# Performance work log

Hardware: AMD Instinct MI355X
Metric: run time of the kernel (lower is better)

The kernel has to match this reference:

```python
import jax, jax.numpy as jnp
import numpy as np

ANCHORS_ALL = jnp.array([[10.,13.],[16.,30.],[33.,23.],[30.,61.],[62.,45.],
                         [59.,119.],[116.,90.],[156.,198.],[373.,326.]], dtype=jnp.float32)
INDICES = jnp.array([0, 1, 2], dtype=jnp.int32)   # anchor indices of level 0
ANCH_LVL = ANCHORS_ALL[0:3]                        # [nA, 2] anchors for this level
STRIDE = 8.0
N_CLS = 80
NA = 3


def _bce_logits(x, t):
    # elementwise binary_cross_entropy_with_logits (same formula as torch)
    return jnp.maximum(x, 0.0) - x * t + jnp.log1p(jnp.exp(-jnp.abs(x)))


def _iou_cxcywh(a, b):
    # a: [..., 4], b: [..., 4] (broadcastable), boxes as (cx, cy, w, h)
    ax1, ax2 = a[..., 0] - a[..., 2] * 0.5, a[..., 0] + a[..., 2] * 0.5
    ay1, ay2 = a[..., 1] - a[..., 3] * 0.5, a[..., 1] + a[..., 3] * 0.5
    bx1, bx2 = b[..., 0] - b[..., 2] * 0.5, b[..., 0] + b[..., 2] * 0.5
    by1, by2 = b[..., 1] - b[..., 3] * 0.5, b[..., 1] + b[..., 3] * 0.5
    iw = jnp.clip(jnp.minimum(ax2, bx2) - jnp.maximum(ax1, bx1), 0.0)
    ih = jnp.clip(jnp.minimum(ay2, by2) - jnp.maximum(ay1, by1), 0.0)
    inter = iw * ih
    union = (ax2 - ax1) * (ay2 - ay1) + (bx2 - bx1) * (by2 - by1) - inter
    return inter / (union + 1e-16)


def setup_inputs() -> dict:
    key = jax.random.key(0)
    ks = jax.random.split(key, 7)
    nB, nA, nH, nW, G = 8, 3, 160, 160, 32
    t_bbox = jax.random.normal(ks[0], (nB, nA, nH, nW, 4), jnp.float32)
    conf_logits = jax.random.normal(ks[1], (nB, nA, nH, nW, 1), jnp.float32)
    cls_logits = jax.random.normal(ks[2], (nB, nA, nH, nW, N_CLS), jnp.float32)
    cxy = jax.random.uniform(ks[3], (nB, G, 2), jnp.float32, 20.0, 1260.0)
    wh = jax.random.uniform(ks[4], (nB, G, 2), jnp.float32, 5.0, 60.0)
    gt_bboxes = jnp.concatenate([cxy, wh], axis=-1)           # cxcywh
    gt_cls = jax.random.randint(ks[5], (nB, G), 0, N_CLS, jnp.int32)
    gt_mask = jax.random.uniform(ks[6], (nB, G)) < 0.8        # padded-GT validity
    return dict(t_bbox=t_bbox, conf_logits=conf_logits, cls_logits=cls_logits,
                gt_bboxes=gt_bboxes, gt_cls=gt_cls, gt_mask=gt_mask)


def reference(t_bbox, conf_logits, cls_logits, gt_bboxes, gt_cls, gt_mask):
    nB, nA, nH, nW, _ = t_bbox.shape
    N = nA * nH * nW
    # ---- bbox decode (torch does this on a detached copy) ----
    sig = jax.nn.sigmoid(jax.lax.stop_gradient(t_bbox))
    yv, xv = jnp.meshgrid(jnp.arange(nH), jnp.arange(nW), indexing='ij')
    grid = jnp.stack([xv, yv], axis=-1).astype(jnp.float32).reshape(1, 1, nH, nW, 2)
    p_xy = (sig[..., 0:2] * 2.0 - 0.5 + grid) * STRIDE
    p_wh = (sig[..., 2:4] * 2.0) ** 2 * ANCH_LVL.reshape(1, nA, 1, 1, 2)
    p_bbox = jnp.concatenate([p_xy, p_wh], axis=-1).reshape(nB, N, 4)
    p_conf = jax.nn.sigmoid(jax.lax.stop_gradient(conf_logits))       # [nB,nA,nH,nW,1]
    p_cls = jax.nn.sigmoid(jax.lax.stop_gradient(cls_logits))
    cls_score = jnp.max(p_cls, axis=-1, keepdims=True)
    cls_idx = jnp.argmax(p_cls, axis=-1).reshape(nB, N)
    score = (p_conf * cls_score).reshape(nB, N)
    # ---- per-GT best-anchor matching (vectorized over [nB, G]) ----
    gw, gh = gt_bboxes[..., 2], gt_bboxes[..., 3]
    aw, ah = ANCHORS_ALL[:, 0], ANCHORS_ALL[:, 1]
    inter = jnp.minimum(gw[..., None], aw) * jnp.minimum(gh[..., None], ah)
    union = (gw * gh)[..., None] + aw * ah - inter
    anch_idx = jnp.argmax(inter / (union + 1e-16), axis=-1)           # [nB,G]
    matched = jnp.any(anch_idx[..., None] == INDICES, axis=-1)
    valid = gt_mask & matched
    ta = (anch_idx % NA).astype(jnp.int32)
    ti = jnp.clip((gt_bboxes[..., 0] / STRIDE).astype(jnp.int32), 0, nW - 1)
    tj = jnp.clip((gt_bboxes[..., 1] / STRIDE).astype(jnp.int32), 0, nH - 1)
    b_idx = jnp.arange(nB)[:, None]
    t_bb = t_bbox[b_idx, ta, tj, ti]       # [nB,G,4]
    t_cl = cls_logits[b_idx, ta, tj, ti]   # [nB,G,C]
    tgt_xy = ((gt_bboxes[..., 0:2] / STRIDE) % 1.0 + 0.5) / 2.0
    tgt_wh = jnp.sqrt(gt_bboxes[..., 2:4] / ANCH_LVL[ta]) / 2.0
    vm = valid.astype(t_bbox.dtype)
    loss_xy = jnp.sum(vm * jnp.sum(_bce_logits(t_bb[..., 0:2], tgt_xy), axis=-1))
    loss_wh = jnp.sum(vm * jnp.sum(_bce_logits(t_bb[..., 2:4], tgt_wh), axis=-1))
    onehot = jax.nn.one_hot(gt_cls, N_CLS, dtype=t_bbox.dtype)
    loss_cls = jnp.sum(vm * jnp.mean(_bce_logits(t_cl, onehot), axis=-1))
    # ---- objectness target: max IoU of every decoded box with the GTs ----
    ious = _iou_cxcywh(p_bbox[:, :, None, :], gt_bboxes[:, None, :, :])  # [nB,N,G]
    ious = jnp.where(gt_mask[:, None, :], ious, -1.0)
    has_gt = jnp.any(gt_mask, axis=-1)
    tconf = jnp.where(has_gt[:, None], jnp.max(ious, axis=-1), 0.0)
    tconf = tconf.reshape(nB, nA, nH, nW, 1)
    loss_conf = jnp.sum(_bce_logits(conf_logits, tconf))
    loss = (loss_xy + loss_wh + loss_conf + loss_cls) / nB
    return p_bbox, cls_idx, score, loss
```

## Files before the change

kernel.cpp:

```cpp
#include <hip/hip_runtime.h>

#define NB 8
#define NA 3
#define NH 160
#define NW 160
#define NCLS 80
#define NGT 32
#define NPB (NA * NH * NW)
#define TOTAL (NB * NPB)
#define OFF_CLSIDX (TOTAL * 4)
#define OFF_SCORE  (TOTAL * 5)
#define OFF_LOSS   (TOTAL * 6)

__device__ float g_acc;

__device__ __forceinline__ float det_sigmoid(float x) { return 1.0f / (1.0f + expf(-x)); }
__device__ __forceinline__ float det_bce(float x, float t) {
    return fmaxf(x, 0.0f) - x * t + log1pf(expf(-fabsf(x)));
}
__device__ __forceinline__ float det_aw3(int a) { return a == 0 ? 10.0f : (a == 1 ? 16.0f : 33.0f); }
__device__ __forceinline__ float det_ah3(int a) { return a == 0 ? 13.0f : (a == 1 ? 30.0f : 23.0f); }

__device__ __forceinline__ bool det_mask_is_u8(const void* p) {
    const unsigned int* w = (const unsigned int*)p;
    unsigned int acc = 0;
#pragma unroll
    for (int k = 0; k < 64; k++) acc |= (w[k] & 0xFFFFFF00u);
    return acc != 0;
}
__device__ __forceinline__ bool det_mask_at(const void* p, bool u8mode, int idx) {
    return u8mode ? (((const unsigned char*)p)[idx] != 0)
                  : (((const int*)p)[idx] != 0);
}

__global__ void det_zero_k() { g_acc = 0.0f; }

__global__ void det_gt_k(const float* __restrict__ t_bbox,
                         const float* __restrict__ cls_logits,
                         const float* __restrict__ gt_bboxes,
                         const int* __restrict__ gt_cls,
                         const void* __restrict__ gt_mask) {
    __shared__ int s_u8;
    if (threadIdx.x == 0) s_u8 = det_mask_is_u8(gt_mask) ? 1 : 0;
    __syncthreads();
    bool u8mode = (s_u8 != 0);

    int t = threadIdx.x;
    int b = t >> 5;
    int g = t & 31;
    float4 gtb = ((const float4*)gt_bboxes)[b * NGT + g];
    float cx = gtb.x, cy = gtb.y, gw = gtb.z, gh = gtb.w;

    const float aw9[9] = {10.f,16.f,33.f,30.f,62.f,59.f,116.f,156.f,373.f};
    const float ah9[9] = {13.f,30.f,23.f,61.f,45.f,119.f,90.f,198.f,326.f};
    float garea = gw * gh;
    int aidx = 0;
    float best = -1.0f;
#pragma unroll
    for (int k = 0; k < 9; k++) {
        float inter = fminf(gw, aw9[k]) * fminf(gh, ah9[k]);
        float uni = garea + aw9[k] * ah9[k] - inter;
        float r = inter / (uni + 1e-16f);
        if (r > best) { best = r; aidx = k; }
    }
    bool valid = det_mask_at(gt_mask, u8mode, b * NGT + g) && (aidx < NA);
    int ta = aidx % NA;
    int ti = min(max((int)(cx * 0.125f), 0), NW - 1);
    int tj = min(max((int)(cy * 0.125f), 0), NH - 1);
    size_t cell = ((size_t)(b * NA + ta) * NH + tj) * NW + ti;

    float4 tb = ((const float4*)t_bbox)[cell];
    float fx = cx * 0.125f; fx -= floorf(fx);
    float fy = cy * 0.125f; fy -= floorf(fy);
    float tx = (fx + 0.5f) * 0.5f;
    float ty = (fy + 0.5f) * 0.5f;
    float tw = sqrtf(gw / det_aw3(ta)) * 0.5f;
    float th = sqrtf(gh / det_ah3(ta)) * 0.5f;

    float l = det_bce(tb.x, tx) + det_bce(tb.y, ty) +
              det_bce(tb.z, tw) + det_bce(tb.w, th);

    const float4* cl = (const float4*)(cls_logits + cell * NCLS);
    int tc = gt_cls[b * NGT + g];
    float lc = 0.0f;
#pragma unroll
    for (int c4 = 0; c4 < NCLS / 4; c4++) {
        float4 v = cl[c4];
        int c = c4 * 4;
        lc += det_bce(v.x, (c + 0 == tc) ? 1.0f : 0.0f);
        lc += det_bce(v.y, (c + 1 == tc) ? 1.0f : 0.0f);
        lc += det_bce(v.z, (c + 2 == tc) ? 1.0f : 0.0f);
        lc += det_bce(v.w, (c + 3 == tc) ? 1.0f : 0.0f);
    }
    l += lc * (1.0f / NCLS);
    if (valid) atomicAdd(&g_acc, l);
}

__global__ __launch_bounds__(256) void det_main_k(
    const float* __restrict__ t_bbox,
    const float* __restrict__ conf_logits,
    const float* __restrict__ cls_logits,
    const float* __restrict__ gt_bboxes,
    const void* __restrict__ gt_mask,
    float* __restrict__ out) {
    __shared__ float s_x1[NGT], s_y1[NGT], s_x2[NGT], s_y2[NGT], s_ar[NGT];
    __shared__ float s_m[NGT];
    __shared__ float s_part[4];
    __shared__ int s_u8;

    int gid = blockIdx.x * 256 + threadIdx.x;
    int b = gid / NPB;
    int r = gid % NPB;

    if (threadIdx.x == 0) s_u8 = det_mask_is_u8(gt_mask) ? 1 : 0;
    __syncthreads();
    if (threadIdx.x < NGT) {
        int g = threadIdx.x;
        float4 gtb = ((const float4*)gt_bboxes)[b * NGT + g];
        s_x1[g] = gtb.x - gtb.z * 0.5f;
        s_x2[g] = gtb.x + gtb.z * 0.5f;
        s_y1[g] = gtb.y - gtb.w * 0.5f;
        s_y2[g] = gtb.y + gtb.w * 0.5f;
        s_ar[g] = gtb.z * gtb.w;
        s_m[g]  = det_mask_at(gt_mask, s_u8 != 0, b * NGT + g) ? 1.0f : 0.0f;
    }
    __syncthreads();

    int a   = r / (NH * NW);
    int rem = r % (NH * NW);
    int j   = rem / NW;
    int i   = rem % NW;

    float4 tb = ((const float4*)t_bbox)[gid];
    float s0 = det_sigmoid(tb.x), s1 = det_sigmoid(tb.y);
    float s2 = det_sigmoid(tb.z), s3 = det_sigmoid(tb.w);
    float px = (s0 * 2.0f - 0.5f + (float)i) * 8.0f;
    float py = (s1 * 2.0f - 0.5f + (float)j) * 8.0f;
    float sw = s2 * 2.0f, sh = s3 * 2.0f;
    float pw = sw * sw * det_aw3(a);
    float ph = sh * sh * det_ah3(a);
    float4 pb; pb.x = px; pb.y = py; pb.z = pw; pb.w = ph;
    ((float4*)out)[gid] = pb;

    const float4* cl = (const float4*)(cls_logits + (size_t)gid * NCLS);
    float mx = -1e30f;
    int mi = 0;
#pragma unroll
    for (int c4 = 0; c4 < NCLS / 4; c4++) {
        float4 v = cl[c4];
        int c = c4 * 4;
        if (v.x > mx) { mx = v.x; mi = c + 0; }
        if (v.y > mx) { mx = v.y; mi = c + 1; }
        if (v.z > mx) { mx = v.z; mi = c + 2; }
        if (v.w > mx) { mx = v.w; mi = c + 3; }
    }
    float confl = conf_logits[gid];
    float score = det_sigmoid(confl) * det_sigmoid(mx);
    out[OFF_CLSIDX + gid] = (float)mi;
    out[OFF_SCORE  + gid] = score;

    float px1 = px - pw * 0.5f, px2 = px + pw * 0.5f;
    float py1 = py - ph * 0.5f, py2 = py + ph * 0.5f;
    float parea = pw * ph;
    float maxiou = 0.0f;
#pragma unroll
    for (int g = 0; g < NGT; g++) {
        float iw = fmaxf(fminf(px2, s_x2[g]) - fmaxf(px1, s_x1[g]), 0.0f);
        float ih = fmaxf(fminf(py2, s_y2[g]) - fmaxf(py1, s_y1[g]), 0.0f);
        float inter = iw * ih;
        float uni = parea + s_ar[g] - inter;
        float iou = inter / (uni + 1e-16f);
        maxiou = fmaxf(maxiou, (s_m[g] != 0.0f) ? iou : 0.0f);
    }

    float lconf = det_bce(confl, maxiou);
#pragma unroll
    for (int off = 32; off > 0; off >>= 1) lconf += __shfl_down(lconf, off, 64);
    int wid = threadIdx.x >> 6, lane = threadIdx.x & 63;
    if (lane == 0) s_part[wid] = lconf;
    __syncthreads();
    if (threadIdx.x == 0)
        atomicAdd(&g_acc, s_part[0] + s_part[1] + s_part[2] + s_part[3]);
}

__global__ void det_fin_k(float* __restrict__ out) {
    out[OFF_LOSS] = g_acc * (1.0f / NB);
}

extern "C" void kernel_launch(void* const* d_in, const int* in_sizes, int n_in,
                              void* d_out, int out_size, void* d_ws, size_t ws_size,
                              hipStream_t stream) {
    (void)in_sizes; (void)n_in; (void)out_size; (void)d_ws; (void)ws_size;
    const float* t_bbox      = (const float*)d_in[0];
    const float* conf_logits = (const float*)d_in[1];
    const float* cls_logits  = (const float*)d_in[2];
    const float* gt_bboxes   = (const float*)d_in[3];
    const int*   gt_cls      = (const int*)d_in[4];
    const void*  gt_mask     = (const void*)d_in[5];
    float* out = (float*)d_out;

    det_zero_k<<<1, 1, 0, stream>>>();
    det_gt_k<<<1, 256, 0, stream>>>(t_bbox, cls_logits, gt_bboxes, gt_cls, gt_mask);
    det_main_k<<<TOTAL / 256, 256, 0, stream>>>(t_bbox, conf_logits, cls_logits,
                                                gt_bboxes, gt_mask, out);
    det_fin_k<<<1, 1, 0, stream>>>(out);
}
```

Baseline: 345.7 us.

## Split class argmax into separate kernel with four threads per cell

Moves the per-cell class argmax and score out of the bbox/IoU kernel into a new kernel where four threads cooperatively scan one cell's 80 logits and reduce with cross-lane shuffles. This is meant to make the big cls_logits read more coalesced and to separate the memory-heavy scan from the compute-heavy IoU loop. It adds a kernel launch and a tie-break rule that picks the lowest index on equal values.

```diff
diff --git a/kernel.cpp b/kernel.cpp
--- a/kernel.cpp
+++ b/kernel.cpp
@@ -96,10 +96,9 @@
     if (valid) atomicAdd(&g_acc, l);
 }
 
-__global__ __launch_bounds__(256) void det_main_k(
+__global__ __launch_bounds__(256) void det_bbox_k(
     const float* __restrict__ t_bbox,
     const float* __restrict__ conf_logits,
-    const float* __restrict__ cls_logits,
     const float* __restrict__ gt_bboxes,
     const void* __restrict__ gt_mask,
     float* __restrict__ out) {
@@ -142,23 +141,6 @@
     float4 pb; pb.x = px; pb.y = py; pb.z = pw; pb.w = ph;
     ((float4*)out)[gid] = pb;
 
-    const float4* cl = (const float4*)(cls_logits + (size_t)gid * NCLS);
-    float mx = -1e30f;
-    int mi = 0;
-#pragma unroll
-    for (int c4 = 0; c4 < NCLS / 4; c4++) {
-        float4 v = cl[c4];
-        int c = c4 * 4;
-        if (v.x > mx) { mx = v.x; mi = c + 0; }
-        if (v.y > mx) { mx = v.y; mi = c + 1; }
-        if (v.z > mx) { mx = v.z; mi = c + 2; }
-        if (v.w > mx) { mx = v.w; mi = c + 3; }
-    }
-    float confl = conf_logits[gid];
-    float score = det_sigmoid(confl) * det_sigmoid(mx);
-    out[OFF_CLSIDX + gid] = (float)mi;
-    out[OFF_SCORE  + gid] = score;
-
     float px1 = px - pw * 0.5f, px2 = px + pw * 0.5f;
     float py1 = py - ph * 0.5f, py2 = py + ph * 0.5f;
     float parea = pw * ph;
@@ -173,7 +155,7 @@
         maxiou = fmaxf(maxiou, (s_m[g] != 0.0f) ? iou : 0.0f);
     }
 
-    float lconf = det_bce(confl, maxiou);
+    float lconf = det_bce(conf_logits[gid], maxiou);
 #pragma unroll
     for (int off = 32; off > 0; off >>= 1) lconf += __shfl_down(lconf, off, 64);
     int wid = threadIdx.x >> 6, lane = threadIdx.x & 63;
@@ -181,6 +163,39 @@
     __syncthreads();
     if (threadIdx.x == 0)
         atomicAdd(&g_acc, s_part[0] + s_part[1] + s_part[2] + s_part[3]);
+}
+
+__global__ __launch_bounds__(256) void det_cls_k(
+    const float* __restrict__ conf_logits,
+    const float* __restrict__ cls_logits,
+    float* __restrict__ out) {
+    int t = blockIdx.x * 256 + threadIdx.x;
+    int cell = t >> 2;
+    int q = t & 3;
+    const float4* cl = (const float4*)(cls_logits + (size_t)cell * NCLS);
+    float mx = -1e30f;
+    int mi = 0;
+#pragma unroll
+    for (int k = 0; k < 5; k++) {
+        int c4 = q + (k << 2);
+        float4 v = cl[c4];
+        int c = c4 << 2;
+        if (v.x > mx) { mx = v.x; mi = c + 0; }
+        if (v.y > mx) { mx = v.y; mi = c + 1; }
+        if (v.z > mx) { mx = v.z; mi = c + 2; }
+        if (v.w > mx) { mx = v.w; mi = c + 3; }
+    }
+#pragma unroll
+    for (int s = 1; s < 4; s <<= 1) {
+        float ov = __shfl_xor(mx, s, 64);
+        int   oi = __shfl_xor(mi, s, 64);
+        if (ov > mx || (ov == mx && oi < mi)) { mx = ov; mi = oi; }
+    }
+    if (q == 0) {
+        float score = det_sigmoid(conf_logits[cell]) * det_sigmoid(mx);
+        out[OFF_CLSIDX + cell] = (float)mi;
+        out[OFF_SCORE  + cell] = score;
+    }
 }
 
 __global__ void det_fin_k(float* __restrict__ out) {
@@ -201,7 +216,8 @@
 
     det_zero_k<<<1, 1, 0, stream>>>();
     det_gt_k<<<1, 256, 0, stream>>>(t_bbox, cls_logits, gt_bboxes, gt_cls, gt_mask);
-    det_main_k<<<TOTAL / 256, 256, 0, stream>>>(t_bbox, conf_logits, cls_logits,
+    det_bbox_k<<<TOTAL / 256, 256, 0, stream>>>(t_bbox, conf_logits,
                                                 gt_bboxes, gt_mask, out);
+    det_cls_k<<<(TOTAL * 4) / 256, 256, 0, stream>>>(conf_logits, cls_logits, out);
     det_fin_k<<<1, 1, 0, stream>>>(out);
 }
```

Result: no change. 351.1 us (+1.6%).

## Stage class logits through LDS with coalesced loads for argmax

Applied to the files above, without the earlier changes.

Each thread used to read its own 320-byte class row, which gives strided, uncoalesced global loads. Now each wavefront loads 16-cell tiles of class logits into padded shared memory with contiguous float4 loads. Four lanes per cell then compute partial argmaxes and combine them with xor shuffles. The cost is extra LDS traffic, more __syncthreads barriers inside the loop, and a tie-break rule that prefers the lower index.

```diff
diff --git a/kernel.cpp b/kernel.cpp
--- a/kernel.cpp
+++ b/kernel.cpp
@@ -12,6 +12,9 @@
 #define OFF_SCORE  (TOTAL * 5)
 #define OFF_LOSS   (TOTAL * 6)
 
+#define F4_PER_ROW 20
+#define LDS_ROW_F4 21
+
 __device__ float g_acc;
 
 __device__ __forceinline__ float det_sigmoid(float x) { return 1.0f / (1.0f + expf(-x)); }
@@ -103,19 +106,22 @@
     const float* __restrict__ gt_bboxes,
     const void* __restrict__ gt_mask,
     float* __restrict__ out) {
+    __shared__ float4 s_cls[4][16 * LDS_ROW_F4];
     __shared__ float s_x1[NGT], s_y1[NGT], s_x2[NGT], s_y2[NGT], s_ar[NGT];
     __shared__ float s_m[NGT];
     __shared__ float s_part[4];
     __shared__ int s_u8;
 
-    int gid = blockIdx.x * 256 + threadIdx.x;
+    int tid = threadIdx.x;
+    int blockCell = blockIdx.x * 256;
+    int gid = blockCell + tid;
     int b = gid / NPB;
     int r = gid % NPB;
 
-    if (threadIdx.x == 0) s_u8 = det_mask_is_u8(gt_mask) ? 1 : 0;
-    __syncthreads();
-    if (threadIdx.x < NGT) {
-        int g = threadIdx.x;
+    if (tid == 0) s_u8 = det_mask_is_u8(gt_mask) ? 1 : 0;
+    __syncthreads();
+    if (tid < NGT) {
+        int g = tid;
         float4 gtb = ((const float4*)gt_bboxes)[b * NGT + g];
         s_x1[g] = gtb.x - gtb.z * 0.5f;
         s_x2[g] = gtb.x + gtb.z * 0.5f;
@@ -142,23 +148,6 @@
     float4 pb; pb.x = px; pb.y = py; pb.z = pw; pb.w = ph;
     ((float4*)out)[gid] = pb;
 
-    const float4* cl = (const float4*)(cls_logits + (size_t)gid * NCLS);
-    float mx = -1e30f;
-    int mi = 0;
-#pragma unroll
-    for (int c4 = 0; c4 < NCLS / 4; c4++) {
-        float4 v = cl[c4];
-        int c = c4 * 4;
-        if (v.x > mx) { mx = v.x; mi = c + 0; }
-        if (v.y > mx) { mx = v.y; mi = c + 1; }
-        if (v.z > mx) { mx = v.z; mi = c + 2; }
-        if (v.w > mx) { mx = v.w; mi = c + 3; }
-    }
-    float confl = conf_logits[gid];
-    float score = det_sigmoid(confl) * det_sigmoid(mx);
-    out[OFF_CLSIDX + gid] = (float)mi;
-    out[OFF_SCORE  + gid] = score;
-
     float px1 = px - pw * 0.5f, px2 = px + pw * 0.5f;
     float py1 = py - ph * 0.5f, py2 = py + ph * 0.5f;
     float parea = pw * ph;
@@ -173,14 +162,62 @@
         maxiou = fmaxf(maxiou, (s_m[g] != 0.0f) ? iou : 0.0f);
     }
 
+    float confl = conf_logits[gid];
+    float sconf = det_sigmoid(confl);
     float lconf = det_bce(confl, maxiou);
 #pragma unroll
     for (int off = 32; off > 0; off >>= 1) lconf += __shfl_down(lconf, off, 64);
-    int wid = threadIdx.x >> 6, lane = threadIdx.x & 63;
-    if (lane == 0) s_part[wid] = lconf;
-    __syncthreads();
-    if (threadIdx.x == 0)
+    int w = tid >> 6, l = tid & 63;
+    if (l == 0) s_part[w] = lconf;
+    __syncthreads();
+    if (tid == 0)
         atomicAdd(&g_acc, s_part[0] + s_part[1] + s_part[2] + s_part[3]);
+
+    int cl_ = l >> 2;
+    int q   = l & 3;
+    const float4* g4 = (const float4*)cls_logits;
+    int wbase = blockCell + w * 64;
+
+#pragma unroll
+    for (int it = 0; it < 4; ++it) {
+        int tileCell = wbase + it * 16;
+        size_t f4base = (size_t)tileCell * F4_PER_ROW;
+        __syncthreads();
+#pragma unroll
+        for (int k = 0; k < 5; ++k) {
+            int f = k * 64 + l;
+            float4 v = g4[f4base + f];
+            int rr = f / F4_PER_ROW;
+            int cc = f - rr * F4_PER_ROW;
+            s_cls[w][rr * LDS_ROW_F4 + cc] = v;
+        }
+        __syncthreads();
+
+        float mx = -1e30f;
+        int mi = 0;
+#pragma unroll
+        for (int k = 0; k < 5; ++k) {
+            int col = q * 5 + k;
+            float4 v = s_cls[w][cl_ * LDS_ROW_F4 + col];
+            int c = col * 4;
+            if (v.x > mx) { mx = v.x; mi = c + 0; }
+            if (v.y > mx) { mx = v.y; mi = c + 1; }
+            if (v.z > mx) { mx = v.z; mi = c + 2; }
+            if (v.w > mx) { mx = v.w; mi = c + 3; }
+        }
+#pragma unroll
+        for (int s = 1; s < 4; s <<= 1) {
+            float ov = __shfl_xor(mx, s, 64);
+            int   oi = __shfl_xor(mi, s, 64);
+            if (ov > mx || (ov == mx && oi < mi)) { mx = ov; mi = oi; }
+        }
+        float sc = __shfl(sconf, it * 16 + cl_, 64);
+        if (q == 0) {
+            int cellg = tileCell + cl_;
+            out[OFF_CLSIDX + cellg] = (float)mi;
+            out[OFF_SCORE  + cellg] = sc * det_sigmoid(mx);
+        }
+    }
 }
 
 __global__ void det_fin_k(float* __restrict__ out) {
```

After: 329.6 us. -4.7%, faster.
